# Optimization experiments

Hardware: AMD Instinct MI355X
Metric: run time of the kernel (lower is better)

Reference implementation:

```python
import jax, jax.numpy as jnp
import numpy as np

# Model dims (scaled Mistral-style decoder)
L = 2        # layers
D = 2048     # d_model
H = 16       # query heads
HK = 4       # kv heads (GQA)
HD = 128     # head dim
F = 8192     # SwiGLU hidden
V = 32000    # vocab
R = 64       # LoRA rank
BATCH = 16
S = 128
BLK = 64             # NF4 quant blocksize
SCALE = 128.0 / 64.0  # lora_alpha / r
THETA = 10000.0
EPS = 1e-5

# bitsandbytes NF4 codebook (16 levels)
NF4 = jnp.array([-1.0, -0.6961928009986877, -0.5250730514526367, -0.39491748809814453,
                 -0.28444138169288635, -0.18477343022823334, -0.09105003625154495, 0.0,
                 0.07958029955625534, 0.16093020141124725, 0.24611230194568634,
                 0.33791524171829224, 0.44070982933044434, 0.5626170039176941,
                 0.7229568362236023, 1.0], dtype=jnp.float32)


def _dequant(codes, absmax):
    # codes: [out, in] int codes 0..15; absmax: [out, in//BLK] per-block scale
    o, i = codes.shape
    w = NF4[codes].reshape(o, i // BLK, BLK) * absmax[:, :, None]
    return w.reshape(o, i)


def _qlinear(x, codes, absmax, A, Bm):
    # fused NF4 dequant + GEMM + LoRA delta: y = x W^T + scale * (x A^T) B^T
    return x @ _dequant(codes, absmax).T + SCALE * ((x @ A.T) @ Bm.T)


def _rms(x, w):
    return x * jax.lax.rsqrt(jnp.mean(x * x, axis=-1, keepdims=True) + EPS) * w


def _rope(x):
    # x: [B, S, heads, HD]; rotate-half RoPE
    half = HD // 2
    inv = 1.0 / (THETA ** (jnp.arange(half, dtype=jnp.float32) / half))
    ang = jnp.arange(x.shape[1], dtype=jnp.float32)[:, None] * inv[None, :]  # [S, half]
    cos = jnp.cos(ang)[None, :, None, :]
    sin = jnp.sin(ang)[None, :, None, :]
    x1, x2 = x[..., :half], x[..., half:]
    return jnp.concatenate([x1 * cos - x2 * sin, x2 * cos + x1 * sin], axis=-1)


def reference(input_ids, attention_mask, embed, attn_norm_w, mlp_norm_w, final_norm_w,
              q_codes, q_absmax, q_A, q_B, k_codes, k_absmax, k_A, k_B,
              v_codes, v_absmax, v_A, v_B, o_codes, o_absmax, o_A, o_B,
              gate_codes, gate_absmax, gate_A, gate_B, up_codes, up_absmax, up_A, up_B,
              down_codes, down_absmax, down_A, down_B):
    b, s = input_ids.shape
    h = embed[input_ids]  # [B, S, D]
    causal = jnp.tril(jnp.ones((s, s), dtype=bool))
    keep = causal[None, None, :, :] & (attention_mask[:, None, None, :] > 0)
    bias = jnp.where(keep, 0.0, -1e9).astype(h.dtype)
    for l in range(L):
        x = _rms(h, attn_norm_w[l])
        q = _qlinear(x, q_codes[l], q_absmax[l], q_A[l], q_B[l]).reshape(b, s, H, HD)
        k = _qlinear(x, k_codes[l], k_absmax[l], k_A[l], k_B[l]).reshape(b, s, HK, HD)
        v = _qlinear(x, v_codes[l], v_absmax[l], v_A[l], v_B[l]).reshape(b, s, HK, HD)
        q = _rope(q)
        k = _rope(k)
        k = jnp.repeat(k, H // HK, axis=2)  # GQA expand
        v = jnp.repeat(v, H // HK, axis=2)
        scores = jnp.einsum('bqhd,bkhd->bhqk', q, k) / jnp.sqrt(jnp.float32(HD)) + bias
        attn = jax.nn.softmax(scores, axis=-1)
        ctx = jnp.einsum('bhqk,bkhd->bqhd', attn, v).reshape(b, s, D)
        h = h + _qlinear(ctx, o_codes[l], o_absmax[l], o_A[l], o_B[l])
        x = _rms(h, mlp_norm_w[l])
        g = _qlinear(x, gate_codes[l], gate_absmax[l], gate_A[l], gate_B[l])
        u = _qlinear(x, up_codes[l], up_absmax[l], up_A[l], up_B[l])
        h = h + _qlinear(jax.nn.silu(g) * u, down_codes[l], down_absmax[l], down_A[l], down_B[l])
    h = _rms(h, final_norm_w)
    # last-token pooling: gather hidden state at sum(mask)-1 (normalized=False)
    seq_len = jnp.sum(attention_mask, axis=1) - 1
    return h[jnp.arange(b), seq_len]


def setup_inputs() -> dict:
    key = jax.random.key(0)
    ks = iter(jax.random.split(key, 64))
    def codes(shape):
        return jax.random.randint(next(ks), shape, 0, 16, dtype=jnp.int32)
    def absm(o, i):
        return jax.random.uniform(next(ks), (L, o, i // BLK), dtype=jnp.float32) * 0.05
    def lora(o, i):
        A = jax.random.normal(next(ks), (L, R, i), dtype=jnp.float32) * 0.02
        Bm = jax.random.normal(next(ks), (L, o, R), dtype=jnp.float32) * 0.02
        return A, Bm
    inp = {
        'input_ids': jax.random.randint(next(ks), (BATCH, S), 0, V, dtype=jnp.int32),
        'attention_mask': jnp.ones((BATCH, S), dtype=jnp.int32),
        'embed': jax.random.normal(next(ks), (V, D), dtype=jnp.float32) * 0.02,
        'attn_norm_w': jnp.ones((L, D), jnp.float32),
        'mlp_norm_w': jnp.ones((L, D), jnp.float32),
        'final_norm_w': jnp.ones((D,), jnp.float32),
    }
    dims = {'q': (D, D), 'k': (HK * HD, D), 'v': (HK * HD, D), 'o': (D, D),
            'gate': (F, D), 'up': (F, D), 'down': (D, F)}
    for name, (o, i) in dims.items():
        A, Bm = lora(o, i)
        inp[f'{name}_codes'] = codes((L, o, i))
        inp[f'{name}_absmax'] = absm(o, i)
        inp[f'{name}_A'] = A
        inp[f'{name}_B'] = Bm
    return inp
```

## Files before the change

### kernel.cpp

```cpp
#include <hip/hip_runtime.h>
#include <stdint.h>

#define D_ 2048
#define H_ 16
#define HK_ 4
#define F_ 8192
#define R_ 64
#define NTOK_ 2048
#define EPS_ 1e-5f

typedef unsigned short u16;
typedef short short8 __attribute__((ext_vector_type(8)));
typedef float f32x4 __attribute__((ext_vector_type(4)));

__constant__ float NF4_TAB[16] = {
  -1.0f, -0.6961928009986877f, -0.5250730514526367f, -0.39491748809814453f,
  -0.28444138169288635f, -0.18477343022823334f, -0.09105003625154495f, 0.0f,
  0.07958029955625534f, 0.16093020141124725f, 0.24611230194568634f, 0.33791524171829224f,
  0.44070982933044434f, 0.5626170039176941f, 0.7229568362236023f, 1.0f };

static __device__ __forceinline__ float b2f(u16 u){ return __uint_as_float(((unsigned)u)<<16); }
static __device__ __forceinline__ u16 f2b(float f){
  unsigned u = __float_as_uint(f);
  return (u16)((u + 0x7fffu + ((u>>16)&1u)) >> 16);
}

__global__ void k_embed(const int* __restrict__ ids, const float* __restrict__ embed,
                        float* __restrict__ h){
  int tok = blockIdx.x;
  int id  = ids[tok];
  const float4* src = (const float4*)(embed + (size_t)id * D_);
  float4* dst = (float4*)(h + (size_t)tok * D_);
  for (int i = threadIdx.x; i < D_/4; i += 256) dst[i] = src[i];
}

__global__ void k_rms(const float* __restrict__ h, const float* __restrict__ w,
                      u16* __restrict__ xb){
  __shared__ float red[4];
  int row = blockIdx.x, t = threadIdx.x;
  const float* hr = h + (size_t)row * D_;
  float ss = 0.f;
  for (int i = t; i < D_; i += 256){ float v = hr[i]; ss += v*v; }
  #pragma unroll
  for (int m = 32; m; m >>= 1) ss += __shfl_xor(ss, m, 64);
  if ((t & 63) == 0) red[t >> 6] = ss;
  __syncthreads();
  float sc = rsqrtf((red[0]+red[1]+red[2]+red[3]) * (1.0f/D_) + EPS_);
  for (int i = t; i < D_; i += 256) xb[(size_t)row*D_ + i] = f2b(hr[i]*sc*w[i]);
}

__global__ __launch_bounds__(256) void k_fold(const int* __restrict__ codes,
      const float* __restrict__ absmax, const float* __restrict__ Amat,
      const float* __restrict__ Bmat, u16* __restrict__ W, int O, int I){
  __shared__ u16  A_l[64*128];
  __shared__ float Bt_l[64*132];
  __shared__ float nf4s[16];
  int t = threadIdx.x;
  int n0 = blockIdx.y*128, k0 = blockIdx.x*128;
  if (t < 16) nf4s[t] = NF4_TAB[t];
  #pragma unroll
  for (int it = 0; it < 8; ++it){
    int fi = it*256 + t;
    int r = fi >> 5, c4 = fi & 31;
    float4 v = *(const float4*)(Amat + (size_t)r*I + k0 + c4*4);
    uint2 p; p.x = (unsigned)f2b(v.x) | ((unsigned)f2b(v.y)<<16);
    p.y = (unsigned)f2b(v.z) | ((unsigned)f2b(v.w)<<16);
    *(uint2*)&A_l[r*128 + c4*4] = p;
  }
  #pragma unroll
  for (int it = 0; it < 8; ++it){
    int fi = it*256 + t; int nl = fi >> 4, r4 = fi & 15;
    float4 v = *(const float4*)(Bmat + (size_t)(n0+nl)*R_ + r4*4);
    Bt_l[(r4*4+0)*132 + nl] = v.x; Bt_l[(r4*4+1)*132 + nl] = v.y;
    Bt_l[(r4*4+2)*132 + nl] = v.z; Bt_l[(r4*4+3)*132 + nl] = v.w;
  }
  __syncthreads();
  int tk = t & 15, tn = t >> 4;
  float acc[8][8];
  #pragma unroll
  for (int j = 0; j < 8; ++j)
    #pragma unroll
    for (int q = 0; q < 8; ++q) acc[j][q] = 0.f;
  for (int r = 0; r < 64; ++r){
    short8 a8 = *(const short8*)&A_l[r*128 + tk*8];
    float av[8];
    #pragma unroll
    for (int q = 0; q < 8; ++q) av[q] = b2f((u16)a8[q]);
    float4 b0 = *(const float4*)&Bt_l[r*132 + tn*8];
    float4 b1 = *(const float4*)&Bt_l[r*132 + tn*8 + 4];
    float bv[8] = {b0.x,b0.y,b0.z,b0.w,b1.x,b1.y,b1.z,b1.w};
    #pragma unroll
    for (int j = 0; j < 8; ++j)
      #pragma unroll
      for (int q = 0; q < 8; ++q) acc[j][q] += bv[j]*av[q];
  }
  int kb = k0 + tk*8;
  #pragma unroll
  for (int j = 0; j < 8; ++j){
    int n = n0 + tn*8 + j;
    float am = absmax[(size_t)n*(I>>6) + (kb>>6)];
    int4 c0 = *(const int4*)(codes + (size_t)n*I + kb);
    int4 c1 = *(const int4*)(codes + (size_t)n*I + kb + 4);
    u16 o[8];
    o[0]=f2b(nf4s[c0.x&15]*am + 2.0f*acc[j][0]);
    o[1]=f2b(nf4s[c0.y&15]*am + 2.0f*acc[j][1]);
    o[2]=f2b(nf4s[c0.z&15]*am + 2.0f*acc[j][2]);
    o[3]=f2b(nf4s[c0.w&15]*am + 2.0f*acc[j][3]);
    o[4]=f2b(nf4s[c1.x&15]*am + 2.0f*acc[j][4]);
    o[5]=f2b(nf4s[c1.y&15]*am + 2.0f*acc[j][5]);
    o[6]=f2b(nf4s[c1.z&15]*am + 2.0f*acc[j][6]);
    o[7]=f2b(nf4s[c1.w&15]*am + 2.0f*acc[j][7]);
    uint4 pk;
    pk.x=(unsigned)o[0]|((unsigned)o[1]<<16); pk.y=(unsigned)o[2]|((unsigned)o[3]<<16);
    pk.z=(unsigned)o[4]|((unsigned)o[5]<<16); pk.w=(unsigned)o[6]|((unsigned)o[7]<<16);
    *(uint4*)(W + (size_t)n*I + kb) = pk;
  }
}

template<int EPI>
__global__ __launch_bounds__(256,3) void k_gemm(const u16* __restrict__ A,
      const u16* __restrict__ B, float* __restrict__ Cf, u16* __restrict__ C0,
      u16* __restrict__ C1, u16* __restrict__ C2, int M, int N, int K){
  __shared__ u16 SA[2][128*32];
  __shared__ u16 SB[2][128*32];
  int t = threadIdx.x;
  int n0 = blockIdx.x*128, m0 = blockIdx.y*128;
  int w = t >> 6, lane = t & 63;
  int mw = (w >> 1)*64, nw = (w & 1)*64;
  int lr = lane & 15, lg = lane >> 4;
  f32x4 acc[4][4];
  #pragma unroll
  for (int mt = 0; mt < 4; ++mt)
    #pragma unroll
    for (int nt = 0; nt < 4; ++nt) acc[mt][nt] = (f32x4){0.f,0.f,0.f,0.f};
  const u16* Ag = A + (size_t)(m0 + (t>>2))*K + (t&3)*8;
  const u16* Bg = B + (size_t)(n0 + (t>>2))*K + (t&3)*8;
  int t8 = t*8;
  int niter = K >> 5;

  uint4 ra0, ra1, rb0, rb1;
  uint4 sa0, sa1, sb0, sb1;
  auto gload = [&](int it, uint4& a0, uint4& a1, uint4& b0, uint4& b1){
    int kb = it*32;
    a0 = *(const uint4*)(Ag + kb);
    a1 = *(const uint4*)(Ag + (size_t)64*K + kb);
    b0 = *(const uint4*)(Bg + kb);
    b1 = *(const uint4*)(Bg + (size_t)64*K + kb);
  };
  gload(0, ra0, ra1, rb0, rb1);
  gload(1, sa0, sa1, sb0, sb1);

  auto step = [&](int buf, uint4& a0, uint4& a1, uint4& b0, uint4& b1, int pf){
    *(uint4*)&SA[buf][t8]        = a0;
    *(uint4*)&SA[buf][2048 + t8] = a1;
    *(uint4*)&SB[buf][t8]        = b0;
    *(uint4*)&SB[buf][2048 + t8] = b1;
    __builtin_amdgcn_s_waitcnt(0xC07F);
    __builtin_amdgcn_s_barrier();
    gload(pf, a0, a1, b0, b1);
    short8 af[4], bf_[4];
    #pragma unroll
    for (int mt = 0; mt < 4; ++mt) af[mt]  = *(const short8*)&SA[buf][(mw + mt*16 + lr)*32 + lg*8];
    #pragma unroll
    for (int nt = 0; nt < 4; ++nt) bf_[nt] = *(const short8*)&SB[buf][(nw + nt*16 + lr)*32 + lg*8];
    #pragma unroll
    for (int mt = 0; mt < 4; ++mt)
      #pragma unroll
      for (int nt = 0; nt < 4; ++nt)
        acc[mt][nt] = __builtin_amdgcn_mfma_f32_16x16x32_bf16(af[mt], bf_[nt], acc[mt][nt], 0, 0, 0);
  };

  for (int k = 0; k < niter; k += 2){
    step(0, ra0, ra1, rb0, rb1, (k+2 < niter) ? k+2 : k);
    step(1, sa0, sa1, sb0, sb1, (k+3 < niter) ? k+3 : k+1);
  }

  u16* cb_ = C0; int ldc = N; int coff = n0;
  if (EPI == 2){
    if (n0 < 2048)      { cb_ = C0; ldc = 2048; coff = n0; }
    else if (n0 < 2560) { cb_ = C1; ldc = 512;  coff = n0 - 2048; }
    else                { cb_ = C2; ldc = 512;  coff = n0 - 2560; }
  }
  if (EPI == 3){
    if (n0 < 512)       { cb_ = C1; ldc = 512;  coff = n0; }
    else                { cb_ = C2; ldc = 512;  coff = n0 - 512; }
  }
  #pragma unroll
  for (int mt = 0; mt < 4; ++mt)
    #pragma unroll
    for (int nt = 0; nt < 4; ++nt){
      int cl = nw + nt*16 + lr;
      #pragma unroll
      for (int rg = 0; rg < 4; ++rg){
        int row = m0 + mw + mt*16 + lg*4 + rg;
        float v = acc[mt][nt][rg];
        if (EPI == 1) Cf[(size_t)row*N + n0 + cl] += v;
        else          cb_[(size_t)row*ldc + coff + cl] = f2b(v);
      }
    }
}

template<int OUT>
__global__ __launch_bounds__(256) void k_skinny(const u16* __restrict__ A,
      const u16* __restrict__ B, float* __restrict__ Hf, u16* __restrict__ Cb,
      const int* __restrict__ rows, int N, int K, int Kc){
  int w = threadIdx.x >> 6, lane = threadIdx.x & 63;
  int lr = lane & 15, lg = lane >> 4;
  int n0 = blockIdx.x*64 + w*16;
  int kbase = blockIdx.y * Kc;
  f32x4 acc = (f32x4){0.f,0.f,0.f,0.f};
  const u16* Ap = A + (size_t)lr*K + kbase + lg*8;
  const u16* Bp = B + (size_t)(n0 + lr)*K + kbase + lg*8;
  for (int k = 0; k < Kc; k += 32){
    short8 a = *(const short8*)(Ap + k);
    short8 b = *(const short8*)(Bp + k);
    acc = __builtin_amdgcn_mfma_f32_16x16x32_bf16(a, b, acc, 0, 0, 0);
  }
  #pragma unroll
  for (int rg = 0; rg < 4; ++rg){
    int m = lg*4 + rg;
    if (OUT == 0) Cb[(size_t)m*N + n0 + lr] = f2b(acc[rg]);
    else          atomicAdd(&Hf[(size_t)rows[m]*D_ + n0 + lr], acc[rg]);
  }
}

__global__ void k_rows(const int* __restrict__ mask, int* __restrict__ rows){
  int b = threadIdx.x;
  if (b < 16){
    int c = 0;
    for (int i = 0; i < 128; ++i) c += (mask[b*128+i] > 0);
    rows[b] = b*128 + c - 1;
  }
}

__global__ void k_gather16(const u16* __restrict__ xb, const int* __restrict__ rows,
                           u16* __restrict__ xq){
  int m = blockIdx.x, t = threadIdx.x;
  *(uint4*)(xq + (size_t)m*2048 + t*8) =
      *(const uint4*)(xb + (size_t)rows[m]*2048 + t*8);
}

__global__ void k_rms16(const float* __restrict__ h, const float* __restrict__ w,
                        const int* __restrict__ rows, u16* __restrict__ xq){
  __shared__ float red[4];
  int m = blockIdx.x, t = threadIdx.x;
  const float* hr = h + (size_t)rows[m] * D_;
  float ss = 0.f;
  for (int i = t; i < D_; i += 256){ float v = hr[i]; ss += v*v; }
  #pragma unroll
  for (int mm = 32; mm; mm >>= 1) ss += __shfl_xor(ss, mm, 64);
  if ((t & 63) == 0) red[t >> 6] = ss;
  __syncthreads();
  float sc = rsqrtf((red[0]+red[1]+red[2]+red[3]) * (1.0f/D_) + EPS_);
  for (int i = t; i < D_; i += 256) xq[(size_t)m*D_ + i] = f2b(hr[i]*sc*w[i]);
}

__global__ void k_rope(u16* __restrict__ x, int nh){
  int i = blockIdx.x*256 + threadIdx.x;
  int d = i & 63; int rem = i >> 6; int hh = rem % nh; int tok = rem / nh;
  int s = tok & 127;
  size_t base = (size_t)tok*nh*128 + hh*128 + d;
  float x1 = b2f(x[base]), x2 = b2f(x[base+64]);
  float inv = exp2f(-(float)d * 0.20762050581352868f);
  float ang = (float)s * inv;
  float sn = sinf(ang), cs = cosf(ang);
  x[base]      = f2b(x1*cs - x2*sn);
  x[base+64]   = f2b(x2*cs + x1*sn);
}

__global__ void k_rope16(u16* __restrict__ x, const int* __restrict__ rows){
  int i = blockIdx.x*256 + threadIdx.x;
  int d = i & 63; int hh = (i >> 6) & 15; int m = i >> 10;
  int s = rows[m] & 127;
  size_t base = (size_t)m*2048 + hh*128 + d;
  float x1 = b2f(x[base]), x2 = b2f(x[base+64]);
  float inv = exp2f(-(float)d * 0.20762050581352868f);
  float ang = (float)s * inv;
  float sn = sinf(ang), cs = cosf(ang);
  x[base]      = f2b(x1*cs - x2*sn);
  x[base+64]   = f2b(x2*cs + x1*sn);
}

__global__ __launch_bounds__(256) void k_attn(const u16* __restrict__ q,
      const u16* __restrict__ kk, const u16* __restrict__ vv,
      const int* __restrict__ mask, u16* __restrict__ ctx){
  __shared__ u16 QP[128*128];
  __shared__ u16 KV[128*128];
  int b = blockIdx.y, h = blockIdx.x;
  int t = threadIdx.x, w = t >> 6, lane = t & 63;
  int lr = lane & 15, lg = lane >> 4;
  #pragma unroll
  for (int it = 0; it < 8; ++it){
    int fi = it*256 + t; int s = fi >> 4, c8 = fi & 15;
    *(uint4*)&QP[s*128 + c8*8] = *(const uint4*)(q  + (size_t)(b*128+s)*2048 + h*128 + c8*8);
    *(uint4*)&KV[s*128 + c8*8] = *(const uint4*)(kk + (size_t)(b*128+s)*512 + (h>>2)*128 + c8*8);
  }
  __syncthreads();
  f32x4 sac[2][8];
  #pragma unroll
  for (int mt = 0; mt < 2; ++mt)
    #pragma unroll
    for (int nt = 0; nt < 8; ++nt) sac[mt][nt] = (f32x4){0.f,0.f,0.f,0.f};
  for (int ks = 0; ks < 128; ks += 32){
    short8 a[2], bb[8];
    #pragma unroll
    for (int mt = 0; mt < 2; ++mt) a[mt] = *(const short8*)&QP[(w*32 + mt*16 + lr)*128 + ks + lg*8];
    #pragma unroll
    for (int nt = 0; nt < 8; ++nt) bb[nt] = *(const short8*)&KV[(nt*16 + lr)*128 + ks + lg*8];
    #pragma unroll
    for (int mt = 0; mt < 2; ++mt)
      #pragma unroll
      for (int nt = 0; nt < 8; ++nt)
        sac[mt][nt] = __builtin_amdgcn_mfma_f32_16x16x32_bf16(a[mt], bb[nt], sac[mt][nt], 0, 0, 0);
  }
  const float NEG = -1e9f, scl = 0.08838834764831845f;
  float mbias[8];
  #pragma unroll
  for (int nt = 0; nt < 8; ++nt) mbias[nt] = (mask[b*128 + nt*16 + lr] > 0) ? 0.f : NEG;
  #pragma unroll
  for (int mt = 0; mt < 2; ++mt)
    #pragma unroll
    for (int rg = 0; rg < 4; ++rg){
      int row = w*32 + mt*16 + lg*4 + rg;
      float vvv[8]; float mx = -3e38f;
      #pragma unroll
      for (int nt = 0; nt < 8; ++nt){
        int col = nt*16 + lr;
        float s_ = sac[mt][nt][rg]*scl + ((col <= row) ? mbias[nt] : NEG);
        vvv[nt] = s_; mx = fmaxf(mx, s_);
      }
      #pragma unroll
      for (int m_ = 1; m_ < 16; m_ <<= 1) mx = fmaxf(mx, __shfl_xor(mx, m_, 64));
      float sum = 0.f;
      #pragma unroll
      for (int nt = 0; nt < 8; ++nt){ vvv[nt] = __expf(vvv[nt]-mx); sum += vvv[nt]; }
      #pragma unroll
      for (int m_ = 1; m_ < 16; m_ <<= 1) sum += __shfl_xor(sum, m_, 64);
      float inv = 1.0f/sum;
      #pragma unroll
      for (int nt = 0; nt < 8; ++nt) QP[row*128 + nt*16 + lr] = f2b(vvv[nt]*inv);
    }
  __syncthreads();
  #pragma unroll
  for (int it = 0; it < 8; ++it){
    int fi = it*256 + t; int s = fi >> 4, c8 = fi & 15;
    u16 tmp[8];
    *(uint4*)tmp = *(const uint4*)(vv + (size_t)(b*128+s)*512 + (h>>2)*128 + c8*8);
    #pragma unroll
    for (int j = 0; j < 8; ++j) KV[(c8*8+j)*128 + s] = tmp[j];
  }
  __syncthreads();
  f32x4 oac[2][8];
  #pragma unroll
  for (int mt = 0; mt < 2; ++mt)
    #pragma unroll
    for (int nt = 0; nt < 8; ++nt) oac[mt][nt] = (f32x4){0.f,0.f,0.f,0.f};
  for (int ks = 0; ks < 128; ks += 32){
    short8 a[2], bb[8];
    #pragma unroll
    for (int mt = 0; mt < 2; ++mt) a[mt] = *(const short8*)&QP[(w*32 + mt*16 + lr)*128 + ks + lg*8];
    #pragma unroll
    for (int nt = 0; nt < 8; ++nt) bb[nt] = *(const short8*)&KV[(nt*16 + lr)*128 + ks + lg*8];
    #pragma unroll
    for (int mt = 0; mt < 2; ++mt)
      #pragma unroll
      for (int nt = 0; nt < 8; ++nt)
        oac[mt][nt] = __builtin_amdgcn_mfma_f32_16x16x32_bf16(a[mt], bb[nt], oac[mt][nt], 0, 0, 0);
  }
  #pragma unroll
  for (int mt = 0; mt < 2; ++mt)
    #pragma unroll
    for (int nt = 0; nt < 8; ++nt)
      #pragma unroll
      for (int rg = 0; rg < 4; ++rg){
        int row = w*32 + mt*16 + lg*4 + rg;
        int col = nt*16 + lr;
        ctx[(size_t)(b*128+row)*2048 + h*128 + col] = f2b(oac[mt][nt][rg]);
      }
}

__global__ void k_attn1(const u16* __restrict__ qc, const u16* __restrict__ kk,
      const u16* __restrict__ vv, const int* __restrict__ mask,
      const int* __restrict__ rows, u16* __restrict__ out){
  __shared__ float ps[128];
  __shared__ float red2[2];
  int h = blockIdx.x, b = blockIdx.y, t = threadIdx.x;
  int pos = rows[b] & 127;
  const u16* qrow = qc + (size_t)b*2048 + h*128;
  const u16* krow = kk + (size_t)(b*128 + t)*512 + (h>>2)*128;
  float acc = 0.f;
  #pragma unroll
  for (int d0 = 0; d0 < 128; d0 += 8){
    short8 qa = *(const short8*)(qrow + d0);
    short8 ka = *(const short8*)(krow + d0);
    #pragma unroll
    for (int j = 0; j < 8; ++j) acc += b2f((u16)qa[j]) * b2f((u16)ka[j]);
  }
  bool keep = (t <= pos) && (mask[b*128 + t] > 0);
  float s_ = keep ? acc * 0.08838834764831845f : -1e9f;
  float mx = s_;
  #pragma unroll
  for (int m_ = 1; m_ < 64; m_ <<= 1) mx = fmaxf(mx, __shfl_xor(mx, m_, 64));
  if ((t & 63) == 0) red2[t >> 6] = mx;
  __syncthreads();
  mx = fmaxf(red2[0], red2[1]);
  float p = __expf(s_ - mx);
  float sum = p;
  #pragma unroll
  for (int m_ = 1; m_ < 64; m_ <<= 1) sum += __shfl_xor(sum, m_, 64);
  __syncthreads();
  if ((t & 63) == 0) red2[t >> 6] = sum;
  __syncthreads();
  float inv = 1.f / (red2[0] + red2[1]);
  ps[t] = p * inv;
  __syncthreads();
  float o = 0.f;
  const u16* vbase = vv + (size_t)b*128*512 + (h>>2)*128 + t;
  for (int s = 0; s < 128; s += 4){
    o += ps[s]   * b2f(vbase[(size_t)(s  )*512]);
    o += ps[s+1] * b2f(vbase[(size_t)(s+1)*512]);
    o += ps[s+2] * b2f(vbase[(size_t)(s+2)*512]);
    o += ps[s+3] * b2f(vbase[(size_t)(s+3)*512]);
  }
  out[(size_t)b*2048 + h*128 + t] = f2b(o);
}

__global__ void k_silu(u16* __restrict__ g, const u16* __restrict__ u, int n8){
  int i = blockIdx.x*256 + threadIdx.x;
  if (i >= n8) return;
  u16 gv[8], uv[8];
  *(uint4*)gv = *(const uint4*)(g + (size_t)i*8);
  *(uint4*)uv = *(const uint4*)(u + (size_t)i*8);
  #pragma unroll
  for (int j = 0; j < 8; ++j){
    float x = b2f(gv[j]), y = b2f(uv[j]);
    float s = x / (1.0f + __expf(-x));
    gv[j] = f2b(s*y);
  }
  *(uint4*)(g + (size_t)i*8) = *(uint4*)gv;
}

__global__ void k_final(const float* __restrict__ h, const int* __restrict__ mask,
                        const float* __restrict__ w, float* __restrict__ out){
  __shared__ float red[4]; __shared__ int rowsh;
  int b = blockIdx.x, t = threadIdx.x;
  if (t == 0){
    int c = 0;
    for (int i = 0; i < 128; ++i) c += (mask[b*128+i] > 0);
    rowsh = b*128 + c - 1;
  }
  __syncthreads();
  const float* hr = h + (size_t)rowsh*D_;
  float ss = 0.f;
  for (int i = t; i < D_; i += 256){ float x = hr[i]; ss += x*x; }
  #pragma unroll
  for (int m = 32; m; m >>= 1) ss += __shfl_xor(ss, m, 64);
  if ((t & 63) == 0) red[t >> 6] = ss;
  __syncthreads();
  float sc = rsqrtf((red[0]+red[1]+red[2]+red[3]) * (1.0f/D_) + EPS_);
  for (int i = t; i < D_; i += 256) out[(size_t)b*D_ + i] = hr[i]*sc*w[i];
}

extern "C" void kernel_launch(void* const* d_in, const int* in_sizes, int n_in,
                              void* d_out, int out_size, void* d_ws, size_t ws_size,
                              hipStream_t stream) {
  const int*   ids       = (const int*)  d_in[0];
  const int*   mask      = (const int*)  d_in[1];
  const float* embed     = (const float*)d_in[2];
  const float* attn_norm = (const float*)d_in[3];
  const float* mlp_norm  = (const float*)d_in[4];
  const float* fin_norm  = (const float*)d_in[5];
  struct QW { const int* c; const float* am; const float* A; const float* B; };
  auto qw = [&](int i){ return QW{(const int*)d_in[i], (const float*)d_in[i+1],
                                  (const float*)d_in[i+2], (const float*)d_in[i+3]}; };
  QW Wq = qw(6), Wk = qw(10), Wv = qw(14), Wo = qw(18), Wg = qw(22), Wu = qw(26), Wd = qw(30);

  char* ws = (char*)d_ws;
  float* h  = (float*)(ws);
  u16* xb   = (u16*)(ws + 16777216);
  u16* qb   = (u16*)(ws + 25165824);
  u16* kb_  = (u16*)(ws + 33554432);
  u16* vb   = (u16*)(ws + 35651584);
  u16* gb   = (u16*)(ws + 37748736);
  u16* ub   = (u16*)(ws + 71303168);
  u16* Wb   = (u16*)(ws + 104857600);
  int* rowsi = (int*)(ws + 138412032);
  u16* xq    = (u16*)(ws + 138413056);
  u16* qc    = (u16*)(ws + 138478592);
  u16* cc    = (u16*)(ws + 138544128);
  u16* g16   = (u16*)(ws + 138609664);
  u16* u16b  = (u16*)(ws + 138871808);

  k_embed<<<NTOK_, 256, 0, stream>>>(ids, embed, h);

  for (int l = 0; l < 2; ++l){
    k_rms<<<NTOK_, 256, 0, stream>>>(h, attn_norm + l*D_, xb);
    k_fold<<<dim3(16,16), 256, 0, stream>>>(Wq.c + (size_t)l*D_*D_, Wq.am + (size_t)l*D_*32,
        Wq.A + (size_t)l*R_*D_, Wq.B + (size_t)l*D_*R_, Wb, D_, D_);
    k_fold<<<dim3(16,4), 256, 0, stream>>>(Wk.c + (size_t)l*512*D_, Wk.am + (size_t)l*512*32,
        Wk.A + (size_t)l*R_*D_, Wk.B + (size_t)l*512*R_, Wb + (size_t)2048*D_, 512, D_);
    k_fold<<<dim3(16,4), 256, 0, stream>>>(Wv.c + (size_t)l*512*D_, Wv.am + (size_t)l*512*32,
        Wv.A + (size_t)l*R_*D_, Wv.B + (size_t)l*512*R_, Wb + (size_t)2560*D_, 512, D_);

    if (l == 0){
      k_gemm<2><<<dim3(24,16), 256, 0, stream>>>(xb, Wb, nullptr, qb, kb_, vb, NTOK_, 3072, D_);
      k_rope<<<8192, 256, 0, stream>>>(qb, H_);
      k_rope<<<2048, 256, 0, stream>>>(kb_, HK_);
      k_attn<<<dim3(16,16), 256, 0, stream>>>(qb, kb_, vb, mask, xb);
      k_fold<<<dim3(16,16), 256, 0, stream>>>(Wo.c + (size_t)l*D_*D_, Wo.am + (size_t)l*D_*32,
          Wo.A + (size_t)l*R_*D_, Wo.B + (size_t)l*D_*R_, Wb, D_, D_);
      k_gemm<1><<<dim3(16,16), 256, 0, stream>>>(xb, Wb, h, nullptr, nullptr, nullptr, NTOK_, D_, D_);
      k_rms<<<NTOK_, 256, 0, stream>>>(h, mlp_norm + l*D_, xb);
      k_fold<<<dim3(16,64), 256, 0, stream>>>(Wg.c + (size_t)l*F_*D_, Wg.am + (size_t)l*F_*32,
          Wg.A + (size_t)l*R_*D_, Wg.B + (size_t)l*F_*R_, Wb, F_, D_);
      k_gemm<0><<<dim3(64,16), 256, 0, stream>>>(xb, Wb, nullptr, gb, nullptr, nullptr, NTOK_, F_, D_);
      k_fold<<<dim3(16,64), 256, 0, stream>>>(Wu.c + (size_t)l*F_*D_, Wu.am + (size_t)l*F_*32,
          Wu.A + (size_t)l*R_*D_, Wu.B + (size_t)l*F_*R_, Wb, F_, D_);
      k_gemm<0><<<dim3(64,16), 256, 0, stream>>>(xb, Wb, nullptr, ub, nullptr, nullptr, NTOK_, F_, D_);
      k_silu<<<8192, 256, 0, stream>>>(gb, ub, NTOK_*F_/8);
      k_fold<<<dim3(64,16), 256, 0, stream>>>(Wd.c + (size_t)l*D_*F_, Wd.am + (size_t)l*D_*128,
          Wd.A + (size_t)l*R_*F_, Wd.B + (size_t)l*D_*R_, Wb, D_, F_);
      k_gemm<1><<<dim3(16,16), 256, 0, stream>>>(gb, Wb, h, nullptr, nullptr, nullptr, NTOK_, D_, F_);
    } else {
      k_gemm<3><<<dim3(8,16), 256, 0, stream>>>(xb, Wb + (size_t)2048*D_, nullptr, nullptr,
          kb_, vb, NTOK_, 1024, D_);
      k_rows<<<1, 64, 0, stream>>>(mask, rowsi);
      k_gather16<<<16, 256, 0, stream>>>(xb, rowsi, xq);
      k_skinny<0><<<dim3(32,1), 256, 0, stream>>>(xq, Wb, nullptr, qc, rowsi, D_, D_, D_);
      k_rope16<<<64, 256, 0, stream>>>(qc, rowsi);
      k_rope<<<2048, 256, 0, stream>>>(kb_, HK_);
      k_attn1<<<dim3(16,16), 128, 0, stream>>>(qc, kb_, vb, mask, rowsi, cc);
      k_fold<<<dim3(16,16), 256, 0, stream>>>(Wo.c + (size_t)l*D_*D_, Wo.am + (size_t)l*D_*32,
          Wo.A + (size_t)l*R_*D_, Wo.B + (size_t)l*D_*R_, Wb, D_, D_);
      k_skinny<1><<<dim3(32,1), 256, 0, stream>>>(cc, Wb, h, nullptr, rowsi, D_, D_, D_);
      k_rms16<<<16, 256, 0, stream>>>(h, mlp_norm + l*D_, rowsi, xq);
      k_fold<<<dim3(16,64), 256, 0, stream>>>(Wg.c + (size_t)l*F_*D_, Wg.am + (size_t)l*F_*32,
          Wg.A + (size_t)l*R_*D_, Wg.B + (size_t)l*F_*R_, Wb, F_, D_);
      k_skinny<0><<<dim3(128,1), 256, 0, stream>>>(xq, Wb, nullptr, g16, rowsi, F_, D_, D_);
      k_fold<<<dim3(16,64), 256, 0, stream>>>(Wu.c + (size_t)l*F_*D_, Wu.am + (size_t)l*F_*32,
          Wu.A + (size_t)l*R_*D_, Wu.B + (size_t)l*F_*R_, Wb, F_, D_);
      k_skinny<0><<<dim3(128,1), 256, 0, stream>>>(xq, Wb, nullptr, u16b, rowsi, F_, D_, D_);
      k_silu<<<64, 256, 0, stream>>>(g16, u16b, 16*F_/8);
      k_fold<<<dim3(64,16), 256, 0, stream>>>(Wd.c + (size_t)l*D_*F_, Wd.am + (size_t)l*D_*128,
          Wd.A + (size_t)l*R_*F_, Wd.B + (size_t)l*D_*R_, Wb, D_, F_);
      k_skinny<1><<<dim3(32,4), 256, 0, stream>>>(g16, Wb, h, nullptr, rowsi, D_, F_, D_);
    }
  }
  k_final<<<16, 256, 0, stream>>>(h, mask, fin_norm, (float*)d_out);
}
```

Measured before the change: 1.435 ms.

## Use MFMA for LoRA fold, batch fold launches, fuse SiLU into up-projection epilogue

The LoRA fold kernel now computes B·A with bf16 MFMA instructions on XOR-swizzled shared-memory tiles instead of scalar FMAs, and q/k/v and gate/up folds are each issued as one launch. The SiLU-multiply step is folded into the up-projection epilogue of both the GEMM and the skinny kernel, which removes the separate silu pass and the up-projection buffer. The skinny kernel gathers rows directly instead of running a separate gather kernel, uses compile-time K and two accumulators. The fold's LoRA product loses some precision because A and B are now rounded to bf16, and a second weight buffer is added.

```diff
diff --git a/kernel.cpp b/kernel.cpp
--- a/kernel.cpp
+++ b/kernel.cpp
@@ -49,72 +49,86 @@
   for (int i = t; i < D_; i += 256) xb[(size_t)row*D_ + i] = f2b(hr[i]*sc*w[i]);
 }
 
-__global__ __launch_bounds__(256) void k_fold(const int* __restrict__ codes,
-      const float* __restrict__ absmax, const float* __restrict__ Amat,
-      const float* __restrict__ Bmat, u16* __restrict__ W, int O, int I){
-  __shared__ u16  A_l[64*128];
-  __shared__ float Bt_l[64*132];
+struct FoldSet { const int* c; const float* am; const float* A; const float* Bm; u16* W; };
+
+static __device__ __forceinline__ void fold_tile(const int* __restrict__ codes,
+    const float* __restrict__ absmax, const float* __restrict__ Amat,
+    const float* __restrict__ Bmat, u16* __restrict__ W, int I, int n0, int k0){
+  __shared__ u16 At[128*64];
+  __shared__ u16 Bl[128*64];
   __shared__ float nf4s[16];
   int t = threadIdx.x;
-  int n0 = blockIdx.y*128, k0 = blockIdx.x*128;
   if (t < 16) nf4s[t] = NF4_TAB[t];
   #pragma unroll
   for (int it = 0; it < 8; ++it){
     int fi = it*256 + t;
     int r = fi >> 5, c4 = fi & 31;
     float4 v = *(const float4*)(Amat + (size_t)r*I + k0 + c4*4);
+    int kc0 = c4*4;
+    At[((kc0+0)*64 + r) ^ (((kc0+0)&7)<<3)] = f2b(v.x);
+    At[((kc0+1)*64 + r) ^ (((kc0+1)&7)<<3)] = f2b(v.y);
+    At[((kc0+2)*64 + r) ^ (((kc0+2)&7)<<3)] = f2b(v.z);
+    At[((kc0+3)*64 + r) ^ (((kc0+3)&7)<<3)] = f2b(v.w);
+  }
+  #pragma unroll
+  for (int it = 0; it < 8; ++it){
+    int fi = it*256 + t;
+    int nl = fi >> 4, r4 = fi & 15;
+    float4 v = *(const float4*)(Bmat + (size_t)(n0+nl)*R_ + r4*4);
     uint2 p; p.x = (unsigned)f2b(v.x) | ((unsigned)f2b(v.y)<<16);
     p.y = (unsigned)f2b(v.z) | ((unsigned)f2b(v.w)<<16);
-    *(uint2*)&A_l[r*128 + c4*4] = p;
-  }
-  #pragma unroll
-  for (int it = 0; it < 8; ++it){
-    int fi = it*256 + t; int nl = fi >> 4, r4 = fi & 15;
-    float4 v = *(const float4*)(Bmat + (size_t)(n0+nl)*R_ + r4*4);
-    Bt_l[(r4*4+0)*132 + nl] = v.x; Bt_l[(r4*4+1)*132 + nl] = v.y;
-    Bt_l[(r4*4+2)*132 + nl] = v.z; Bt_l[(r4*4+3)*132 + nl] = v.w;
-  }
-  __syncthreads();
-  int tk = t & 15, tn = t >> 4;
-  float acc[8][8];
-  #pragma unroll
-  for (int j = 0; j < 8; ++j)
-    #pragma unroll
-    for (int q = 0; q < 8; ++q) acc[j][q] = 0.f;
-  for (int r = 0; r < 64; ++r){
-    short8 a8 = *(const short8*)&A_l[r*128 + tk*8];
-    float av[8];
-    #pragma unroll
-    for (int q = 0; q < 8; ++q) av[q] = b2f((u16)a8[q]);
-    float4 b0 = *(const float4*)&Bt_l[r*132 + tn*8];
-    float4 b1 = *(const float4*)&Bt_l[r*132 + tn*8 + 4];
-    float bv[8] = {b0.x,b0.y,b0.z,b0.w,b1.x,b1.y,b1.z,b1.w};
-    #pragma unroll
-    for (int j = 0; j < 8; ++j)
-      #pragma unroll
-      for (int q = 0; q < 8; ++q) acc[j][q] += bv[j]*av[q];
-  }
-  int kb = k0 + tk*8;
-  #pragma unroll
-  for (int j = 0; j < 8; ++j){
-    int n = n0 + tn*8 + j;
-    float am = absmax[(size_t)n*(I>>6) + (kb>>6)];
-    int4 c0 = *(const int4*)(codes + (size_t)n*I + kb);
-    int4 c1 = *(const int4*)(codes + (size_t)n*I + kb + 4);
-    u16 o[8];
-    o[0]=f2b(nf4s[c0.x&15]*am + 2.0f*acc[j][0]);
-    o[1]=f2b(nf4s[c0.y&15]*am + 2.0f*acc[j][1]);
-    o[2]=f2b(nf4s[c0.z&15]*am + 2.0f*acc[j][2]);
-    o[3]=f2b(nf4s[c0.w&15]*am + 2.0f*acc[j][3]);
-    o[4]=f2b(nf4s[c1.x&15]*am + 2.0f*acc[j][4]);
-    o[5]=f2b(nf4s[c1.y&15]*am + 2.0f*acc[j][5]);
-    o[6]=f2b(nf4s[c1.z&15]*am + 2.0f*acc[j][6]);
-    o[7]=f2b(nf4s[c1.w&15]*am + 2.0f*acc[j][7]);
-    uint4 pk;
-    pk.x=(unsigned)o[0]|((unsigned)o[1]<<16); pk.y=(unsigned)o[2]|((unsigned)o[3]<<16);
-    pk.z=(unsigned)o[4]|((unsigned)o[5]<<16); pk.w=(unsigned)o[6]|((unsigned)o[7]<<16);
-    *(uint4*)(W + (size_t)n*I + kb) = pk;
-  }
+    *(uint2*)&Bl[(nl*64 + r4*4) ^ ((nl&7)<<3)] = p;
+  }
+  __syncthreads();
+  int w = t >> 6, lane = t & 63;
+  int lr = lane & 15, lg = lane >> 4;
+  f32x4 acc[2][8];
+  #pragma unroll
+  for (int mt = 0; mt < 2; ++mt)
+    #pragma unroll
+    for (int nt = 0; nt < 8; ++nt) acc[mt][nt] = (f32x4){0.f,0.f,0.f,0.f};
+  #pragma unroll
+  for (int ks = 0; ks < 64; ks += 32){
+    short8 af[2], bf_[8];
+    #pragma unroll
+    for (int mt = 0; mt < 2; ++mt)
+      af[mt] = *(const short8*)&At[((w*32 + mt*16 + lr)*64 + ks + lg*8) ^ ((lr&7)<<3)];
+    #pragma unroll
+    for (int nt = 0; nt < 8; ++nt)
+      bf_[nt] = *(const short8*)&Bl[((nt*16 + lr)*64 + ks + lg*8) ^ ((lr&7)<<3)];
+    #pragma unroll
+    for (int mt = 0; mt < 2; ++mt)
+      #pragma unroll
+      for (int nt = 0; nt < 8; ++nt)
+        acc[mt][nt] = __builtin_amdgcn_mfma_f32_16x16x32_bf16(af[mt], bf_[nt], acc[mt][nt], 0, 0, 0);
+  }
+  int Ib = I >> 6;
+  #pragma unroll
+  for (int mt = 0; mt < 2; ++mt){
+    int kcb = k0 + w*32 + mt*16 + lg*4;
+    int kblk = kcb >> 6;
+    #pragma unroll
+    for (int nt = 0; nt < 8; ++nt){
+      int n = n0 + nt*16 + lr;
+      float am = absmax[(size_t)n*Ib + kblk];
+      int4 c = *(const int4*)(codes + (size_t)n*I + kcb);
+      u16 o0 = f2b(nf4s[c.x&15]*am + 2.0f*acc[mt][nt][0]);
+      u16 o1 = f2b(nf4s[c.y&15]*am + 2.0f*acc[mt][nt][1]);
+      u16 o2 = f2b(nf4s[c.z&15]*am + 2.0f*acc[mt][nt][2]);
+      u16 o3 = f2b(nf4s[c.w&15]*am + 2.0f*acc[mt][nt][3]);
+      uint2 pk; pk.x = (unsigned)o0 | ((unsigned)o1<<16);
+      pk.y = (unsigned)o2 | ((unsigned)o3<<16);
+      *(uint2*)(W + (size_t)n*I + kcb) = pk;
+    }
+  }
+}
+
+__global__ __launch_bounds__(256) void k_fold3(FoldSet a, FoldSet b, FoldSet c,
+                                               int y1, int y2, int I){
+  int y = blockIdx.y;
+  FoldSet s = (y < y1) ? a : (y < y2) ? b : c;
+  int n0 = (y < y1) ? y*128 : (y < y2) ? (y-y1)*128 : (y-y2)*128;
+  fold_tile(s.c, s.am, s.A, s.Bm, s.W, I, n0, blockIdx.x*128);
 }
 
 template<int EPI>
@@ -194,33 +208,52 @@
       for (int rg = 0; rg < 4; ++rg){
         int row = m0 + mw + mt*16 + lg*4 + rg;
         float v = acc[mt][nt][rg];
-        if (EPI == 1) Cf[(size_t)row*N + n0 + cl] += v;
-        else          cb_[(size_t)row*ldc + coff + cl] = f2b(v);
+        if (EPI == 1){
+          Cf[(size_t)row*N + n0 + cl] += v;
+        } else if (EPI == 4){
+          size_t idx = (size_t)row*ldc + coff + cl;
+          float g = b2f(C1[idx]);
+          cb_[idx] = f2b((g/(1.0f+__expf(-g)))*v);
+        } else {
+          cb_[(size_t)row*ldc + coff + cl] = f2b(v);
+        }
       }
     }
 }
 
-template<int OUT>
+template<int OUT, int GA, int KC>
 __global__ __launch_bounds__(256) void k_skinny(const u16* __restrict__ A,
       const u16* __restrict__ B, float* __restrict__ Hf, u16* __restrict__ Cb,
-      const int* __restrict__ rows, int N, int K, int Kc){
+      const int* __restrict__ rows, int N, int K){
   int w = threadIdx.x >> 6, lane = threadIdx.x & 63;
   int lr = lane & 15, lg = lane >> 4;
   int n0 = blockIdx.x*64 + w*16;
-  int kbase = blockIdx.y * Kc;
-  f32x4 acc = (f32x4){0.f,0.f,0.f,0.f};
-  const u16* Ap = A + (size_t)lr*K + kbase + lg*8;
+  int kbase = blockIdx.y * KC;
+  int ar = GA ? rows[lr] : lr;
+  f32x4 ac0 = (f32x4){0.f,0.f,0.f,0.f};
+  f32x4 ac1 = (f32x4){0.f,0.f,0.f,0.f};
+  const u16* Ap = A + (size_t)ar*K + kbase + lg*8;
   const u16* Bp = B + (size_t)(n0 + lr)*K + kbase + lg*8;
-  for (int k = 0; k < Kc; k += 32){
-    short8 a = *(const short8*)(Ap + k);
-    short8 b = *(const short8*)(Bp + k);
-    acc = __builtin_amdgcn_mfma_f32_16x16x32_bf16(a, b, acc, 0, 0, 0);
-  }
+  #pragma unroll 8
+  for (int k = 0; k < KC; k += 64){
+    ac0 = __builtin_amdgcn_mfma_f32_16x16x32_bf16(*(const short8*)(Ap + k),
+            *(const short8*)(Bp + k), ac0, 0, 0, 0);
+    ac1 = __builtin_amdgcn_mfma_f32_16x16x32_bf16(*(const short8*)(Ap + k + 32),
+            *(const short8*)(Bp + k + 32), ac1, 0, 0, 0);
+  }
+  f32x4 acc = ac0 + ac1;
   #pragma unroll
   for (int rg = 0; rg < 4; ++rg){
     int m = lg*4 + rg;
-    if (OUT == 0) Cb[(size_t)m*N + n0 + lr] = f2b(acc[rg]);
-    else          atomicAdd(&Hf[(size_t)rows[m]*D_ + n0 + lr], acc[rg]);
+    if (OUT == 0){
+      Cb[(size_t)m*N + n0 + lr] = f2b(acc[rg]);
+    } else if (OUT == 1){
+      atomicAdd(&Hf[(size_t)rows[m]*D_ + n0 + lr], acc[rg]);
+    } else {
+      size_t idx = (size_t)m*N + n0 + lr;
+      float g = b2f(Cb[idx]);
+      Cb[idx] = f2b((g/(1.0f+__expf(-g)))*acc[rg]);
+    }
   }
 }
 
@@ -231,13 +264,6 @@
     for (int i = 0; i < 128; ++i) c += (mask[b*128+i] > 0);
     rows[b] = b*128 + c - 1;
   }
-}
-
-__global__ void k_gather16(const u16* __restrict__ xb, const int* __restrict__ rows,
-                           u16* __restrict__ xq){
-  int m = blockIdx.x, t = threadIdx.x;
-  *(uint4*)(xq + (size_t)m*2048 + t*8) =
-      *(const uint4*)(xb + (size_t)rows[m]*2048 + t*8);
 }
 
 __global__ void k_rms16(const float* __restrict__ h, const float* __restrict__ w,
@@ -423,21 +449,6 @@
     o += ps[s+3] * b2f(vbase[(size_t)(s+3)*512]);
   }
   out[(size_t)b*2048 + h*128 + t] = f2b(o);
-}
-
-__global__ void k_silu(u16* __restrict__ g, const u16* __restrict__ u, int n8){
-  int i = blockIdx.x*256 + threadIdx.x;
-  if (i >= n8) return;
-  u16 gv[8], uv[8];
-  *(uint4*)gv = *(const uint4*)(g + (size_t)i*8);
-  *(uint4*)uv = *(const uint4*)(u + (size_t)i*8);
-  #pragma unroll
-  for (int j = 0; j < 8; ++j){
-    float x = b2f(gv[j]), y = b2f(uv[j]);
-    float s = x / (1.0f + __expf(-x));
-    gv[j] = f2b(s*y);
-  }
-  *(uint4*)(g + (size_t)i*8) = *(uint4*)gv;
 }
 
 __global__ void k_final(const float* __restrict__ h, const int* __restrict__ mask,
@@ -482,68 +493,79 @@
   u16* kb_  = (u16*)(ws + 33554432);
   u16* vb   = (u16*)(ws + 35651584);
   u16* gb   = (u16*)(ws + 37748736);
-  u16* ub   = (u16*)(ws + 71303168);
   u16* Wb   = (u16*)(ws + 104857600);
   int* rowsi = (int*)(ws + 138412032);
   u16* xq    = (u16*)(ws + 138413056);
   u16* qc    = (u16*)(ws + 138478592);
   u16* cc    = (u16*)(ws + 138544128);
   u16* g16   = (u16*)(ws + 138609664);
-  u16* u16b  = (u16*)(ws + 138871808);
+  u16* Wb2   = (u16*)(ws + 167772160);
+
+  auto fs = [&](QW W_, int l, int O, int I, u16* dst){
+    return FoldSet{ W_.c + (size_t)l*O*I, W_.am + (size_t)l*O*(I>>6),
+                    W_.A + (size_t)l*R_*I, W_.B + (size_t)l*O*R_, dst };
+  };
 
   k_embed<<<NTOK_, 256, 0, stream>>>(ids, embed, h);
 
   for (int l = 0; l < 2; ++l){
     k_rms<<<NTOK_, 256, 0, stream>>>(h, attn_norm + l*D_, xb);
-    k_fold<<<dim3(16,16), 256, 0, stream>>>(Wq.c + (size_t)l*D_*D_, Wq.am + (size_t)l*D_*32,
-        Wq.A + (size_t)l*R_*D_, Wq.B + (size_t)l*D_*R_, Wb, D_, D_);
-    k_fold<<<dim3(16,4), 256, 0, stream>>>(Wk.c + (size_t)l*512*D_, Wk.am + (size_t)l*512*32,
-        Wk.A + (size_t)l*R_*D_, Wk.B + (size_t)l*512*R_, Wb + (size_t)2048*D_, 512, D_);
-    k_fold<<<dim3(16,4), 256, 0, stream>>>(Wv.c + (size_t)l*512*D_, Wv.am + (size_t)l*512*32,
-        Wv.A + (size_t)l*R_*D_, Wv.B + (size_t)l*512*R_, Wb + (size_t)2560*D_, 512, D_);
+    {
+      FoldSet fq = fs(Wq, l, D_, D_, Wb);
+      FoldSet fk = fs(Wk, l, 512, D_, Wb + (size_t)2048*D_);
+      FoldSet fv = fs(Wv, l, 512, D_, Wb + (size_t)2560*D_);
+      k_fold3<<<dim3(16,24), 256, 0, stream>>>(fq, fk, fv, 16, 20, D_);
+    }
 
     if (l == 0){
       k_gemm<2><<<dim3(24,16), 256, 0, stream>>>(xb, Wb, nullptr, qb, kb_, vb, NTOK_, 3072, D_);
       k_rope<<<8192, 256, 0, stream>>>(qb, H_);
       k_rope<<<2048, 256, 0, stream>>>(kb_, HK_);
       k_attn<<<dim3(16,16), 256, 0, stream>>>(qb, kb_, vb, mask, xb);
-      k_fold<<<dim3(16,16), 256, 0, stream>>>(Wo.c + (size_t)l*D_*D_, Wo.am + (size_t)l*D_*32,
-          Wo.A + (size_t)l*R_*D_, Wo.B + (size_t)l*D_*R_, Wb, D_, D_);
+      {
+        FoldSet fo = fs(Wo, l, D_, D_, Wb);
+        k_fold3<<<dim3(16,16), 256, 0, stream>>>(fo, fo, fo, 9999, 9999, D_);
+      }
       k_gemm<1><<<dim3(16,16), 256, 0, stream>>>(xb, Wb, h, nullptr, nullptr, nullptr, NTOK_, D_, D_);
       k_rms<<<NTOK_, 256, 0, stream>>>(h, mlp_norm + l*D_, xb);
-      k_fold<<<dim3(16,64), 256, 0, stream>>>(Wg.c + (size_t)l*F_*D_, Wg.am + (size_t)l*F_*32,
-          Wg.A + (size_t)l*R_*D_, Wg.B + (size_t)l*F_*R_, Wb, F_, D_);
-      k_gemm<0><<<dim3(64,16), 256, 0, stream>>>(xb, Wb, nullptr, gb, nullptr, nullptr, NTOK_, F_, D_);
-      k_fold<<<dim3(16,64), 256, 0, stream>>>(Wu.c + (size_t)l*F_*D_, Wu.am + (size_t)l*F_*32,
-          Wu.A + (size_t)l*R_*D_, Wu.B + (size_t)l*F_*R_, Wb, F_, D_);
-      k_gemm<0><<<dim3(64,16), 256, 0, stream>>>(xb, Wb, nullptr, ub, nullptr, nullptr, NTOK_, F_, D_);
-      k_silu<<<8192, 256, 0, stream>>>(gb, ub, NTOK_*F_/8);
-      k_fold<<<dim3(64,16), 256, 0, stream>>>(Wd.c + (size_t)l*D_*F_, Wd.am + (size_t)l*D_*128,
-          Wd.A + (size_t)l*R_*F_, Wd.B + (size_t)l*D_*R_, Wb, D_, F_);
+      {
+        FoldSet fg = fs(Wg, l, F_, D_, Wb);
+        FoldSet fu = fs(Wu, l, F_, D_, Wb2);
+        k_fold3<<<dim3(16,128), 256, 0, stream>>>(fg, fu, fu, 64, 64, D_);
+      }
+      k_gemm<0><<<dim3(64,16), 256, 0, stream>>>(xb, Wb,  nullptr, gb, nullptr, nullptr, NTOK_, F_, D_);
+      k_gemm<4><<<dim3(64,16), 256, 0, stream>>>(xb, Wb2, nullptr, gb, gb, nullptr, NTOK_, F_, D_);
+      {
+        FoldSet fd = fs(Wd, l, D_, F_, Wb);
+        k_fold3<<<dim3(64,16), 256, 0, stream>>>(fd, fd, fd, 9999, 9999, F_);
+      }
       k_gemm<1><<<dim3(16,16), 256, 0, stream>>>(gb, Wb, h, nullptr, nullptr, nullptr, NTOK_, D_, F_);
     } else {
       k_gemm<3><<<dim3(8,16), 256, 0, stream>>>(xb, Wb + (size_t)2048*D_, nullptr, nullptr,
           kb_, vb, NTOK_, 1024, D_);
       k_rows<<<1, 64, 0, stream>>>(mask, rowsi);
-      k_gather16<<<16, 256, 0, stream>>>(xb, rowsi, xq);
-      k_skinny<0><<<dim3(32,1), 256, 0, stream>>>(xq, Wb, nullptr, qc, rowsi, D_, D_, D_);
+      k_skinny<0,1,2048><<<dim3(32,1), 256, 0, stream>>>(xb, Wb, nullptr, qc, rowsi, D_, D_);
       k_rope16<<<64, 256, 0, stream>>>(qc, rowsi);
       k_rope<<<2048, 256, 0, stream>>>(kb_, HK_);
       k_attn1<<<dim3(16,16), 128, 0, stream>>>(qc, kb_, vb, mask, rowsi, cc);
-      k_fold<<<dim3(16,16), 256, 0, stream>>>(Wo.c + (size_t)l*D_*D_, Wo.am + (size_t)l*D_*32,
-          Wo.A + (size_t)l*R_*D_, Wo.B + (size_t)l*D_*R_, Wb, D_, D_);
-      k_skinny<1><<<dim3(32,1), 256, 0, stream>>>(cc, Wb, h, nullptr, rowsi, D_, D_, D_);
+      {
+        FoldSet fo = fs(Wo, l, D_, D_, Wb);
+        k_fold3<<<dim3(16,16), 256, 0, stream>>>(fo, fo, fo, 9999, 9999, D_);
+      }
+      k_skinny<1,0,2048><<<dim3(32,1), 256, 0, stream>>>(cc, Wb, h, nullptr, rowsi, D_, D_);
       k_rms16<<<16, 256, 0, stream>>>(h, mlp_norm + l*D_, rowsi, xq);
-      k_fold<<<dim3(16,64), 256, 0, stream>>>(Wg.c + (size_t)l*F_*D_, Wg.am + (size_t)l*F_*32,
-          Wg.A + (size_t)l*R_*D_, Wg.B + (size_t)l*F_*R_, Wb, F_, D_);
-      k_skinny<0><<<dim3(128,1), 256, 0, stream>>>(xq, Wb, nullptr, g16, rowsi, F_, D_, D_);
-      k_fold<<<dim3(16,64), 256, 0, stream>>>(Wu.c + (size_t)l*F_*D_, Wu.am + (size_t)l*F_*32,
-          Wu.A + (size_t)l*R_*D_, Wu.B + (size_t)l*F_*R_, Wb, F_, D_);
-      k_skinny<0><<<dim3(128,1), 256, 0, stream>>>(xq, Wb, nullptr, u16b, rowsi, F_, D_, D_);
-      k_silu<<<64, 256, 0, stream>>>(g16, u16b, 16*F_/8);
-      k_fold<<<dim3(64,16), 256, 0, stream>>>(Wd.c + (size_t)l*D_*F_, Wd.am + (size_t)l*D_*128,
-          Wd.A + (size_t)l*R_*F_, Wd.B + (size_t)l*D_*R_, Wb, D_, F_);
-      k_skinny<1><<<dim3(32,4), 256, 0, stream>>>(g16, Wb, h, nullptr, rowsi, D_, F_, D_);
+      {
+        FoldSet fg = fs(Wg, l, F_, D_, Wb);
+        FoldSet fu = fs(Wu, l, F_, D_, Wb2);
+        k_fold3<<<dim3(16,128), 256, 0, stream>>>(fg, fu, fu, 64, 64, D_);
+      }
+      k_skinny<0,0,2048><<<dim3(128,1), 256, 0, stream>>>(xq, Wb,  nullptr, g16, rowsi, F_, D_);
+      k_skinny<3,0,2048><<<dim3(128,1), 256, 0, stream>>>(xq, Wb2, nullptr, g16, rowsi, F_, D_);
+      {
+        FoldSet fd = fs(Wd, l, D_, F_, Wb);
+        k_fold3<<<dim3(64,16), 256, 0, stream>>>(fd, fd, fd, 9999, 9999, F_);
+      }
+      k_skinny<1,0,2048><<<dim3(32,4), 256, 0, stream>>>(g16, Wb, h, nullptr, rowsi, D_, F_);
     }
   }
   k_final<<<16, 256, 0, stream>>>(h, mask, fin_norm, (float*)d_out);
```

Result: slower. 1.473 ms (+2.7%).
